# Kernel tuning notes

Hardware: AMD Instinct MI355X
Metric: run time of the kernel (lower is better)

## Reference

```python
import math
import jax, jax.numpy as jnp
import numpy as np

GRID = 16          # img_size // patch_size = 224 // 14
N_PER_H = 2048     # n_neurons // n_head = 8192 // 4
THETA = 10000.0


def _freqs_2d():
    """2D RoPE phase table, shape (1, 1, GRID*GRID, N_PER_H).
    Layout per position: [h_phases | w_phases | h_phases | w_phases], each half_dim//2 wide.
    """
    dim = N_PER_H
    half = dim // 2
    inv_freq = 1.0 / THETA ** (jnp.arange(0, half, 2, dtype=jnp.float32) / half)  # (half//2,)
    pos = jnp.arange(GRID, dtype=jnp.float32)
    ph = pos[:, None] * inv_freq[None, :]                       # (GRID, half//2)
    ph_h = jnp.broadcast_to(ph[:, None, :], (GRID, GRID, half // 2))
    ph_w = jnp.broadcast_to(ph[None, :, :], (GRID, GRID, half // 2))
    phases = jnp.concatenate([ph_h, ph_w, ph_h, ph_w], axis=-1)  # (GRID, GRID, dim)
    return phases.reshape(1, 1, GRID * GRID, dim)


def _rope(phases, v):
    ang = (phases % 1.0) * (2.0 * math.pi)
    c = jnp.cos(ang)
    s = jnp.sin(ang)
    # interleaved rotation: (-v_odd, v_even) re-interleaved
    v_rot = jnp.stack((-v[..., 1::2], v[..., ::2]), axis=-1).reshape(v.shape)
    return (v * c).astype(v.dtype) + (v_rot * s).astype(v.dtype)


def setup_inputs() -> dict:
    key = jax.random.key(0)
    kq, kk, kv = jax.random.split(key, 3)
    B, H, T, N = 16, 4, 256, N_PER_H
    D = 256
    Q = jax.random.normal(kq, (B, H, T, N), dtype=jnp.float32)
    K = jax.random.normal(kk, (B, H, T, N), dtype=jnp.float32)
    V = jax.random.normal(kv, (B, 1, T, D), dtype=jnp.float32)
    return {"Q": Q, "K": K, "V": V}


def reference(Q, K, V):
    B, H, T, N = Q.shape
    n_patches = GRID * GRID
    freqs = _freqs_2d()[:, :, :n_patches, :N]
    if T == n_patches + 1:  # static-shape branch (CLS token)
        Qr = jnp.concatenate([Q[:, :, :1, :], _rope(freqs, Q[:, :, 1:, :])], axis=2)
        Kr = jnp.concatenate([K[:, :, :1, :], _rope(freqs, K[:, :, 1:, :])], axis=2)
    else:
        f = freqs[:, :, :T, :]
        Qr = _rope(f, Q)
        Kr = _rope(f, K)
    # non-softmax bidirectional attention
    scores = jnp.einsum('bhtn,bhsn->bhts', Qr, Kr) / math.sqrt(N)  # (B,H,T,T)
    return jnp.matmul(scores, V)  # V (B,1,T,D) broadcasts over H -> (B,H,T,D)
```

## Files before the change

kernel.cpp:

```cpp
#include <hip/hip_runtime.h>
#include <hip/hip_bf16.h>

#define T_  256
#define NN_ 2048

typedef short bf16x8 __attribute__((ext_vector_type(8)));
typedef float f32x4  __attribute__((ext_vector_type(4)));
typedef unsigned u32x4 __attribute__((ext_vector_type(4)));

__device__ __forceinline__ unsigned short f2bf(float x) {
    union { float f; unsigned u; } v; v.f = x;
    unsigned r = v.u + 0x7fffu + ((v.u >> 16) & 1u);
    return (unsigned short)(r >> 16);
}
__device__ __forceinline__ float bflo(unsigned w) {
    union { unsigned u; float f; } v; v.u = w << 16; return v.f;
}
__device__ __forceinline__ float bfhi(unsigned w) {
    union { unsigned u; float f; } v; v.u = w & 0xffff0000u; return v.f;
}
__device__ __forceinline__ unsigned pkbf(float lo, float hi) {
    union { __hip_bfloat16 h; unsigned short s; } a, b;
    a.h = __float2bfloat16(lo);
    b.h = __float2bfloat16(hi);
    return (unsigned)a.s | ((unsigned)b.s << 16);
}

__device__ __forceinline__ void gld_lds16(const unsigned short* g, unsigned short* l) {
    __builtin_amdgcn_global_load_lds(
        (const __attribute__((address_space(1))) unsigned int*)g,
        (__attribute__((address_space(3))) unsigned int*)l, 16, 0, 0);
}

__global__ void prep(const float* __restrict__ V, unsigned short* __restrict__ Vt,
                     unsigned* __restrict__ cs) {
    const int tid = threadIdx.x;
    if (blockIdx.x >= 256) {
        int idx = (blockIdx.x - 256) * 256 + tid;
        int p = idx >> 9, f = idx & 511;
        float inv = powf(10000.0f, -(float)f * (1.0f / 512.0f));
        float ph  = (float)p * inv;
        float ang = (ph - floorf(ph)) * 6.28318530717958647692f;
        float s, c;
        sincosf(ang, &s, &c);
        cs[idx] = pkbf(c, s);
        return;
    }
    __shared__ unsigned short Tl[64 * 72];
    const int b  = blockIdx.x >> 4;
    const int s0 = ((blockIdx.x >> 2) & 3) << 6;
    const int d0 = (blockIdx.x & 3) << 6;
    const float* Vb = V + (size_t)b * 65536;
#pragma unroll
    for (int u = 0; u < 4; u++) {
        int lin = u * 256 + tid;
        int srow = lin >> 4, c4 = (lin & 15) << 2;
        float4 v = *(const float4*)(Vb + (size_t)(s0 + srow) * 256 + d0 + c4);
        Tl[(c4 + 0) * 72 + srow] = f2bf(v.x);
        Tl[(c4 + 1) * 72 + srow] = f2bf(v.y);
        Tl[(c4 + 2) * 72 + srow] = f2bf(v.z);
        Tl[(c4 + 3) * 72 + srow] = f2bf(v.w);
    }
    __syncthreads();
    unsigned short* Vtb = Vt + (size_t)b * 65536;
#pragma unroll
    for (int u = 0; u < 2; u++) {
        int lin = u * 256 + tid;
        int drow = lin >> 3, sc8 = (lin & 7) << 3;
        *(uint4*)(Vtb + (size_t)(d0 + drow) * 256 + s0 + sc8) =
            *(const uint4*)(&Tl[drow * 72 + sc8]);
    }
}

#define RSC 0.02209708691207961f

__launch_bounds__(256)
__global__ void rope_cast(const float* __restrict__ Q, const float* __restrict__ K,
                          const unsigned* __restrict__ cs,
                          unsigned short* __restrict__ Qr, unsigned short* __restrict__ Kr) {
    const size_t base = (size_t)blockIdx.x * 256 + threadIdx.x;
#pragma unroll
    for (int j = 0; j < 8; j++) {
        size_t o = base + (size_t)j * 1048576;
        const float* src;
        unsigned short* dst;
        float sc;
        if (j < 4) { src = Q; dst = Qr; sc = RSC; }
        else       { src = K; dst = Kr; sc = 1.0f; o -= 4194304; }
        const int t = (int)((o >> 8) & 255);
        const int w = (int)((o >> 6) & 1);
        const int f = ((int)o & 63) << 3;
        const int p = w ? (t & 15) : (t >> 4);
        const float* qp = src + o * 8;
        float4 q0 = *(const float4*)(qp);
        float4 q1 = *(const float4*)(qp + 4);
        const unsigned* cp = cs + (p << 9) + f;
        uint4 u0 = *(const uint4*)(cp);
        uint4 u1 = *(const uint4*)(cp + 4);
        q0.x *= sc; q0.y *= sc; q0.z *= sc; q0.w *= sc;
        q1.x *= sc; q1.y *= sc; q1.z *= sc; q1.w *= sc;
        u32x4 out;
        out[0] = pkbf(q0.x*bflo(u0.x) - q0.y*bfhi(u0.x),
                      q0.y*bflo(u0.y) + q0.x*bfhi(u0.y));
        out[1] = pkbf(q0.z*bflo(u0.z) - q0.w*bfhi(u0.z),
                      q0.w*bflo(u0.w) + q0.z*bfhi(u0.w));
        out[2] = pkbf(q1.x*bflo(u1.x) - q1.y*bfhi(u1.x),
                      q1.y*bflo(u1.y) + q1.x*bfhi(u1.y));
        out[3] = pkbf(q1.z*bflo(u1.z) - q1.w*bfhi(u1.z),
                      q1.w*bflo(u1.w) + q1.z*bfhi(u1.w));
        __builtin_nontemporal_store(out, (u32x4*)(dst + o * 8));
    }
}

__launch_bounds__(256)
__global__ void gemm1b(const unsigned short* __restrict__ Qr,
                       const unsigned short* __restrict__ Kr,
                       unsigned short* __restrict__ scores) {
    __shared__ __align__(16) unsigned short A[128 * 64];
    __shared__ __align__(16) unsigned short Bt[64 * 64];

    const int tid  = threadIdx.x;
    const int bh   = blockIdx.x & 63;
    const int tile = blockIdx.x >> 6;
    const int ti = (tile >> 2) << 7;
    const int si = (tile & 3) << 6;

    const unsigned short* Qb = Qr + (size_t)bh * (T_ * NN_);
    const unsigned short* Kb = Kr + (size_t)bh * (T_ * NN_);

    const unsigned short* srcA[4]; unsigned short* dstA[4];
    const unsigned short* srcB[2]; unsigned short* dstB[2];
#pragma unroll
    for (int u = 0; u < 4; u++) {
        int lin = u * 256 + tid;
        int row = lin >> 3, cu = lin & 7;
        int scol = cu ^ (row & 7);
        srcA[u] = Qb + (size_t)(ti + row) * NN_ + scol * 8;
        dstA[u] = &A[lin * 8];
    }
#pragma unroll
    for (int u = 0; u < 2; u++) {
        int lin = u * 256 + tid;
        int row = lin >> 3, cu = lin & 7;
        int scol = cu ^ (row & 7);
        srcB[u] = Kb + (size_t)(si + row) * NN_ + scol * 8;
        dstB[u] = &Bt[lin * 8];
    }

    const int wv = tid >> 6, lane = tid & 63;
    const int lr = lane & 15, lg = lane >> 4;
    const int m0 = (wv >> 1) * 64;
    const int n0 = (wv & 1) * 32;

    f32x4 acc[4][2];
#pragma unroll
    for (int i = 0; i < 4; i++)
#pragma unroll
        for (int j = 0; j < 2; j++) acc[i][j] = (f32x4){0.f, 0.f, 0.f, 0.f};

    for (int k0 = 0; k0 < NN_; k0 += 64) {
#pragma unroll
        for (int u = 0; u < 4; u++) gld_lds16(srcA[u] + k0, dstA[u]);
#pragma unroll
        for (int u = 0; u < 2; u++) gld_lds16(srcB[u] + k0, dstB[u]);
        __syncthreads();

#pragma unroll
        for (int kk = 0; kk < 64; kk += 32) {
            bf16x8 af[4], bfr[2];
#pragma unroll
            for (int mi = 0; mi < 4; mi++) {
                int row = m0 + mi * 16 + lr;
                int c   = (kk >> 3) + lg;
                af[mi] = *(const bf16x8*)(&A[row * 64 + ((c ^ (row & 7)) << 3)]);
            }
#pragma unroll
            for (int ni = 0; ni < 2; ni++) {
                int row = n0 + ni * 16 + lr;
                int c   = (kk >> 3) + lg;
                bfr[ni] = *(const bf16x8*)(&Bt[row * 64 + ((c ^ (row & 7)) << 3)]);
            }
#pragma unroll
            for (int mi = 0; mi < 4; mi++)
#pragma unroll
                for (int ni = 0; ni < 2; ni++)
                    acc[mi][ni] = __builtin_amdgcn_mfma_f32_16x16x32_bf16(
                        af[mi], bfr[ni], acc[mi][ni], 0, 0, 0);
        }
        __syncthreads();
    }

    unsigned short* sb = scores + (size_t)bh * (T_ * T_);
#pragma unroll
    for (int mi = 0; mi < 4; mi++) {
        int tr = ti + m0 + mi * 16 + lg * 4;
#pragma unroll
        for (int ni = 0; ni < 2; ni++) {
            int sc = si + n0 + ni * 16 + lr;
#pragma unroll
            for (int r = 0; r < 4; r++)
                sb[(size_t)(tr + r) * 256 + sc] = f2bf(acc[mi][ni][r]);
        }
    }
}

__launch_bounds__(256)
__global__ void gemm2b(const unsigned short* __restrict__ scores,
                       const unsigned short* __restrict__ Vt, float* __restrict__ out) {
    __shared__ __align__(16) unsigned short A[128 * 64];
    __shared__ __align__(16) unsigned short Bt[64 * 64];

    const int tid  = threadIdx.x;
    const int bh   = blockIdx.x & 63;
    const int b    = bh >> 2;
    const int tile = blockIdx.x >> 6;
    const int ti = (tile >> 2) << 7;
    const int d0 = (tile & 3) << 6;

    const unsigned short* Sb  = scores + (size_t)bh * 65536;
    const unsigned short* Vtb = Vt + (size_t)b * 65536;

    const unsigned short* srcA[4]; unsigned short* dstA[4];
    const unsigned short* srcB[2]; unsigned short* dstB[2];
#pragma unroll
    for (int u = 0; u < 4; u++) {
        int lin = u * 256 + tid;
        int row = lin >> 3, cu = lin & 7;
        int scol = cu ^ (row & 7);
        srcA[u] = Sb + (size_t)(ti + row) * 256 + scol * 8;
        dstA[u] = &A[lin * 8];
    }
#pragma unroll
    for (int u = 0; u < 2; u++) {
        int lin = u * 256 + tid;
        int row = lin >> 3, cu = lin & 7;
        int scol = cu ^ (row & 7);
        srcB[u] = Vtb + (size_t)(d0 + row) * 256 + scol * 8;
        dstB[u] = &Bt[lin * 8];
    }

    const int wv = tid >> 6, lane = tid & 63;
    const int lr = lane & 15, lg = lane >> 4;
    const int m0 = (wv >> 1) * 64;
    const int n0 = (wv & 1) * 32;

    f32x4 acc[4][2];
#pragma unroll
    for (int i = 0; i < 4; i++)
#pragma unroll
        for (int j = 0; j < 2; j++) acc[i][j] = (f32x4){0.f, 0.f, 0.f, 0.f};

    for (int k0 = 0; k0 < 256; k0 += 64) {
#pragma unroll
        for (int u = 0; u < 4; u++) gld_lds16(srcA[u] + k0, dstA[u]);
#pragma unroll
        for (int u = 0; u < 2; u++) gld_lds16(srcB[u] + k0, dstB[u]);
        __syncthreads();

#pragma unroll
        for (int kk = 0; kk < 64; kk += 32) {
            bf16x8 af[4], bfr[2];
#pragma unroll
            for (int mi = 0; mi < 4; mi++) {
                int row = m0 + mi * 16 + lr;
                int c   = (kk >> 3) + lg;
                af[mi] = *(const bf16x8*)(&A[row * 64 + ((c ^ (row & 7)) << 3)]);
            }
#pragma unroll
            for (int ni = 0; ni < 2; ni++) {
                int row = n0 + ni * 16 + lr;
                int c   = (kk >> 3) + lg;
                bfr[ni] = *(const bf16x8*)(&Bt[row * 64 + ((c ^ (row & 7)) << 3)]);
            }
#pragma unroll
            for (int mi = 0; mi < 4; mi++)
#pragma unroll
                for (int ni = 0; ni < 2; ni++)
                    acc[mi][ni] = __builtin_amdgcn_mfma_f32_16x16x32_bf16(
                        af[mi], bfr[ni], acc[mi][ni], 0, 0, 0);
        }
        __syncthreads();
    }

    float* ob = out + (size_t)bh * 65536;
#pragma unroll
    for (int mi = 0; mi < 4; mi++) {
        int tr = ti + m0 + mi * 16 + lg * 4;
#pragma unroll
        for (int ni = 0; ni < 2; ni++) {
            int dc = d0 + n0 + ni * 16 + lr;
#pragma unroll
            for (int r = 0; r < 4; r++)
                __builtin_nontemporal_store(acc[mi][ni][r],
                                            ob + (size_t)(tr + r) * 256 + dc);
        }
    }
}

extern "C" void kernel_launch(void* const* d_in, const int* in_sizes, int n_in,
                              void* d_out, int out_size, void* d_ws, size_t ws_size,
                              hipStream_t stream) {
    const float* Q = (const float*)d_in[0];
    const float* K = (const float*)d_in[1];
    const float* V = (const float*)d_in[2];
    float* out = (float*)d_out;

    unsigned* cs = (unsigned*)d_ws;
    unsigned short* scores = (unsigned short*)((char*)d_ws + 32768);
    unsigned short* Vt = (unsigned short*)((char*)d_ws + 32768 + 8388608);
    unsigned short* Qr = (unsigned short*)((char*)d_ws + 16777216);
    unsigned short* Kr = (unsigned short*)((char*)d_ws + 83886080);

    prep<<<dim3(288), dim3(256), 0, stream>>>(V, Vt, cs);
    rope_cast<<<dim3(4096), dim3(256), 0, stream>>>(Q, K, cs, Qr, Kr);
    gemm1b<<<dim3(512), dim3(256), 0, stream>>>(Qr, Kr, scores);
    gemm2b<<<dim3(512), dim3(256), 0, stream>>>(scores, Vt, out);
}
```

Before: 135.5 us.

## Fuse RoPE and bf16 cast into QK GEMM with double-buffered fp32 tiles

Drops the separate rope_cast kernel and its bf16 Qr/Kr round-trip through memory. The QK GEMM now loads fp32 Q/K tiles straight into LDS with double buffering, applies the rotation from an LDS-cached cos/sin table while building MFMA fragments, and applies the 1/sqrt(N) scale at the epilogue. Tiles become 128x128 with 512 threads, 256 blocks. In exchange the GEMM reads twice the bytes per element and does the rotation math in its inner loop, and there are fewer blocks to spread across the CUs.

```diff
diff --git a/kernel.cpp b/kernel.cpp
--- a/kernel.cpp
+++ b/kernel.cpp
@@ -3,6 +3,7 @@
 
 #define T_  256
 #define NN_ 2048
+#define RSC 0.02209708691207961f
 
 typedef short bf16x8 __attribute__((ext_vector_type(8)));
 typedef float f32x4  __attribute__((ext_vector_type(4)));
@@ -25,8 +26,7 @@
     b.h = __float2bfloat16(hi);
     return (unsigned)a.s | ((unsigned)b.s << 16);
 }
-
-__device__ __forceinline__ void gld_lds16(const unsigned short* g, unsigned short* l) {
+__device__ __forceinline__ void gld16(const void* g, void* l) {
     __builtin_amdgcn_global_load_lds(
         (const __attribute__((address_space(1))) unsigned int*)g,
         (__attribute__((address_space(3))) unsigned int*)l, 16, 0, 0);
@@ -72,85 +72,67 @@
     }
 }
 
-#define RSC 0.02209708691207961f
-
-__launch_bounds__(256)
-__global__ void rope_cast(const float* __restrict__ Q, const float* __restrict__ K,
-                          const unsigned* __restrict__ cs,
-                          unsigned short* __restrict__ Qr, unsigned short* __restrict__ Kr) {
-    const size_t base = (size_t)blockIdx.x * 256 + threadIdx.x;
-#pragma unroll
-    for (int j = 0; j < 8; j++) {
-        size_t o = base + (size_t)j * 1048576;
-        const float* src;
-        unsigned short* dst;
-        float sc;
-        if (j < 4) { src = Q; dst = Qr; sc = RSC; }
-        else       { src = K; dst = Kr; sc = 1.0f; o -= 4194304; }
-        const int t = (int)((o >> 8) & 255);
-        const int w = (int)((o >> 6) & 1);
-        const int f = ((int)o & 63) << 3;
-        const int p = w ? (t & 15) : (t >> 4);
-        const float* qp = src + o * 8;
-        float4 q0 = *(const float4*)(qp);
-        float4 q1 = *(const float4*)(qp + 4);
-        const unsigned* cp = cs + (p << 9) + f;
-        uint4 u0 = *(const uint4*)(cp);
-        uint4 u1 = *(const uint4*)(cp + 4);
-        q0.x *= sc; q0.y *= sc; q0.z *= sc; q0.w *= sc;
-        q1.x *= sc; q1.y *= sc; q1.z *= sc; q1.w *= sc;
-        u32x4 out;
-        out[0] = pkbf(q0.x*bflo(u0.x) - q0.y*bfhi(u0.x),
-                      q0.y*bflo(u0.y) + q0.x*bfhi(u0.y));
-        out[1] = pkbf(q0.z*bflo(u0.z) - q0.w*bfhi(u0.z),
-                      q0.w*bflo(u0.w) + q0.z*bfhi(u0.w));
-        out[2] = pkbf(q1.x*bflo(u1.x) - q1.y*bfhi(u1.x),
-                      q1.y*bflo(u1.y) + q1.x*bfhi(u1.y));
-        out[3] = pkbf(q1.z*bflo(u1.z) - q1.w*bfhi(u1.z),
-                      q1.w*bflo(u1.w) + q1.z*bfhi(u1.w));
-        __builtin_nontemporal_store(out, (u32x4*)(dst + o * 8));
-    }
-}
-
-__launch_bounds__(256)
-__global__ void gemm1b(const unsigned short* __restrict__ Qr,
-                       const unsigned short* __restrict__ Kr,
+__launch_bounds__(512)
+__global__ void gemm1f(const float* __restrict__ Q, const float* __restrict__ K,
+                       const unsigned* __restrict__ cs,
                        unsigned short* __restrict__ scores) {
-    __shared__ __align__(16) unsigned short A[128 * 64];
-    __shared__ __align__(16) unsigned short Bt[64 * 64];
-
-    const int tid  = threadIdx.x;
-    const int bh   = blockIdx.x & 63;
-    const int tile = blockIdx.x >> 6;
-    const int ti = (tile >> 2) << 7;
-    const int si = (tile & 3) << 6;
-
-    const unsigned short* Qb = Qr + (size_t)bh * (T_ * NN_);
-    const unsigned short* Kb = Kr + (size_t)bh * (T_ * NN_);
-
-    const unsigned short* srcA[4]; unsigned short* dstA[4];
-    const unsigned short* srcB[2]; unsigned short* dstB[2];
+    __shared__ __align__(16) float rawA[2][128 * 32];
+    __shared__ __align__(16) float rawB[2][128 * 32];
+    __shared__ __align__(16) unsigned csl[16 * 516];
+
+    const int tid = threadIdx.x;
+    const int bh  = blockIdx.x & 63;
+    const int qd  = blockIdx.x >> 6;
+    const int ti  = (qd >> 1) << 7;
+    const int si  = (qd & 1) << 7;
+
+    const float* Qb = Q + (size_t)bh * (T_ * NN_);
+    const float* Kb = K + (size_t)bh * (T_ * NN_);
+
+    const float* srcA[2]; int ldsA[2];
+    const float* srcB[2]; int ldsB[2];
+#pragma unroll
+    for (int u = 0; u < 2; u++) {
+        int lin = u * 512 + tid;
+        int row = lin >> 3, d = lin & 7;
+        int sg  = (d ^ (row & 7)) << 2;
+        srcA[u] = Qb + (size_t)(ti + row) * NN_ + sg;
+        srcB[u] = Kb + (size_t)(si + row) * NN_ + sg;
+        ldsA[u] = lin << 2;
+        ldsB[u] = lin << 2;
+    }
+    const unsigned* csrc[4]; int cdst[4];
 #pragma unroll
     for (int u = 0; u < 4; u++) {
-        int lin = u * 256 + tid;
-        int row = lin >> 3, cu = lin & 7;
-        int scol = cu ^ (row & 7);
-        srcA[u] = Qb + (size_t)(ti + row) * NN_ + scol * 8;
-        dstA[u] = &A[lin * 8];
-    }
-#pragma unroll
-    for (int u = 0; u < 2; u++) {
-        int lin = u * 256 + tid;
-        int row = lin >> 3, cu = lin & 7;
-        int scol = cu ^ (row & 7);
-        srcB[u] = Kb + (size_t)(si + row) * NN_ + scol * 8;
-        dstB[u] = &Bt[lin * 8];
+        int cu = u * 512 + tid;
+        int p = cu >> 7, fg = cu & 127;
+        csrc[u] = cs + (p << 9) + (fg << 2);
+        cdst[u] = p * 516 + (fg << 2);
     }
 
     const int wv = tid >> 6, lane = tid & 63;
     const int lr = lane & 15, lg = lane >> 4;
-    const int m0 = (wv >> 1) * 64;
-    const int n0 = (wv & 1) * 32;
+    const int m0 = (wv >> 2) * 64;
+    const int n0 = (wv & 3) * 32;
+
+    int offA0[4], offA1[4], pAh[4], pAw[4];
+#pragma unroll
+    for (int mi = 0; mi < 4; mi++) {
+        int row = m0 + mi * 16 + lr;
+        int gr  = ti + row;
+        offA0[mi] = row * 32 + ((( 2 * lg    ) ^ (row & 7)) << 2);
+        offA1[mi] = row * 32 + (((2 * lg + 1) ^ (row & 7)) << 2);
+        pAh[mi] = gr >> 4;  pAw[mi] = gr & 15;
+    }
+    int offB0[2], offB1[2], pBh[2], pBw[2];
+#pragma unroll
+    for (int ni = 0; ni < 2; ni++) {
+        int row = n0 + ni * 16 + lr;
+        int gr  = si + row;
+        offB0[ni] = row * 32 + ((( 2 * lg    ) ^ (row & 7)) << 2);
+        offB1[ni] = row * 32 + (((2 * lg + 1) ^ (row & 7)) << 2);
+        pBh[ni] = gr >> 4;  pBw[ni] = gr & 15;
+    }
 
     f32x4 acc[4][2];
 #pragma unroll
@@ -158,37 +140,78 @@
 #pragma unroll
         for (int j = 0; j < 2; j++) acc[i][j] = (f32x4){0.f, 0.f, 0.f, 0.f};
 
-    for (int k0 = 0; k0 < NN_; k0 += 64) {
-#pragma unroll
-        for (int u = 0; u < 4; u++) gld_lds16(srcA[u] + k0, dstA[u]);
-#pragma unroll
-        for (int u = 0; u < 2; u++) gld_lds16(srcB[u] + k0, dstB[u]);
-        __syncthreads();
-
-#pragma unroll
-        for (int kk = 0; kk < 64; kk += 32) {
-            bf16x8 af[4], bfr[2];
-#pragma unroll
-            for (int mi = 0; mi < 4; mi++) {
-                int row = m0 + mi * 16 + lr;
-                int c   = (kk >> 3) + lg;
-                af[mi] = *(const bf16x8*)(&A[row * 64 + ((c ^ (row & 7)) << 3)]);
-            }
-#pragma unroll
-            for (int ni = 0; ni < 2; ni++) {
-                int row = n0 + ni * 16 + lr;
-                int c   = (kk >> 3) + lg;
-                bfr[ni] = *(const bf16x8*)(&Bt[row * 64 + ((c ^ (row & 7)) << 3)]);
-            }
-#pragma unroll
-            for (int mi = 0; mi < 4; mi++)
-#pragma unroll
-                for (int ni = 0; ni < 2; ni++)
-                    acc[mi][ni] = __builtin_amdgcn_mfma_f32_16x16x32_bf16(
-                        af[mi], bfr[ni], acc[mi][ni], 0, 0, 0);
+    auto FRAG = [&](const float* rb, int o0, int o1, int p, int fb) -> bf16x8 {
+        float4 x0 = *(const float4*)(rb + o0);
+        float4 x1 = *(const float4*)(rb + o1);
+        const unsigned* ce = &csl[p * 516 + fb];
+        uint4 e0 = *(const uint4*)(ce);
+        uint4 e1 = *(const uint4*)(ce + 4);
+        union { u32x4 u; bf16x8 h; } o;
+        o.u[0] = pkbf(x0.x * bflo(e0.x) - x0.y * bfhi(e0.x),
+                      x0.y * bflo(e0.y) + x0.x * bfhi(e0.y));
+        o.u[1] = pkbf(x0.z * bflo(e0.z) - x0.w * bfhi(e0.z),
+                      x0.w * bflo(e0.w) + x0.z * bfhi(e0.w));
+        o.u[2] = pkbf(x1.x * bflo(e1.x) - x1.y * bfhi(e1.x),
+                      x1.y * bflo(e1.y) + x1.x * bfhi(e1.y));
+        o.u[3] = pkbf(x1.z * bflo(e1.z) - x1.w * bfhi(e1.z),
+                      x1.w * bflo(e1.w) + x1.z * bfhi(e1.w));
+        return o.h;
+    };
+
+#pragma unroll
+    for (int u = 0; u < 4; u++) gld16(csrc[u], &csl[cdst[u]]);
+#pragma unroll
+    for (int u = 0; u < 2; u++) {
+        gld16(srcA[u], &rawA[0][ldsA[u]]);
+        gld16(srcB[u], &rawB[0][ldsB[u]]);
+    }
+    asm volatile("s_waitcnt vmcnt(0)" ::: "memory");
+    __builtin_amdgcn_s_barrier();
+    asm volatile("" ::: "memory");
+
+#pragma unroll 1
+    for (int k = 0; k < 64; ++k) {
+        const int cur = k & 1;
+        const int kn  = (k < 63) ? (k + 1) : 63;
+#pragma unroll
+        for (int u = 0; u < 2; u++) {
+            gld16(srcA[u] + (kn << 5), &rawA[cur ^ 1][ldsA[u]]);
+            gld16(srcB[u] + (kn << 5), &rawB[cur ^ 1][ldsB[u]]);
         }
-        __syncthreads();
-    }
+        asm volatile("s_waitcnt vmcnt(4)" ::: "memory");
+        __builtin_amdgcn_s_barrier();
+        asm volatile("" ::: "memory");
+
+        const int k0 = k << 5;
+        const int fk = k0 & 511;
+        const int w  = (k0 >> 9) & 1;
+        const int fb = fk + lg * 8;
+
+        bf16x8 afr[4], bfr[2];
+#pragma unroll
+        for (int mi = 0; mi < 4; mi++)
+            afr[mi] = FRAG(&rawA[cur][0], offA0[mi], offA1[mi],
+                           w ? pAw[mi] : pAh[mi], fb);
+#pragma unroll
+        for (int ni = 0; ni < 2; ni++)
+            bfr[ni] = FRAG(&rawB[cur][0], offB0[ni], offB1[ni],
+                           w ? pBw[ni] : pBh[ni], fb);
+
+        __builtin_amdgcn_s_setprio(1);
+#pragma unroll
+        for (int mi = 0; mi < 4; mi++)
+#pragma unroll
+            for (int ni = 0; ni < 2; ni++)
+                acc[mi][ni] = __builtin_amdgcn_mfma_f32_16x16x32_bf16(
+                    afr[mi], bfr[ni], acc[mi][ni], 0, 0, 0);
+        __builtin_amdgcn_s_setprio(0);
+
+        asm volatile("s_waitcnt lgkmcnt(0)" ::: "memory");
+        __builtin_amdgcn_s_barrier();
+        asm volatile("" ::: "memory");
+    }
+
+    asm volatile("s_waitcnt vmcnt(0)" ::: "memory");
 
     unsigned short* sb = scores + (size_t)bh * (T_ * T_);
 #pragma unroll
@@ -199,7 +222,7 @@
             int sc = si + n0 + ni * 16 + lr;
 #pragma unroll
             for (int r = 0; r < 4; r++)
-                sb[(size_t)(tr + r) * 256 + sc] = f2bf(acc[mi][ni][r]);
+                sb[(size_t)(tr + r) * 256 + sc] = f2bf(acc[mi][ni][r] * RSC);
         }
     }
 }
@@ -252,9 +275,9 @@
 
     for (int k0 = 0; k0 < 256; k0 += 64) {
 #pragma unroll
-        for (int u = 0; u < 4; u++) gld_lds16(srcA[u] + k0, dstA[u]);
-#pragma unroll
-        for (int u = 0; u < 2; u++) gld_lds16(srcB[u] + k0, dstB[u]);
+        for (int u = 0; u < 4; u++) gld16(srcA[u] + k0, dstA[u]);
+#pragma unroll
+        for (int u = 0; u < 2; u++) gld16(srcB[u] + k0, dstB[u]);
         __syncthreads();
 
 #pragma unroll
@@ -308,11 +331,8 @@
     unsigned* cs = (unsigned*)d_ws;
     unsigned short* scores = (unsigned short*)((char*)d_ws + 32768);
     unsigned short* Vt = (unsigned short*)((char*)d_ws + 32768 + 8388608);
-    unsigned short* Qr = (unsigned short*)((char*)d_ws + 16777216);
-    unsigned short* Kr = (unsigned short*)((char*)d_ws + 83886080);
 
     prep<<<dim3(288), dim3(256), 0, stream>>>(V, Vt, cs);
-    rope_cast<<<dim3(4096), dim3(256), 0, stream>>>(Q, K, cs, Qr, Kr);
-    gemm1b<<<dim3(512), dim3(256), 0, stream>>>(Qr, Kr, scores);
+    gemm1f<<<dim3(256), dim3(512), 0, stream>>>(Q, K, cs, scores);
     gemm2b<<<dim3(512), dim3(256), 0, stream>>>(scores, Vt, out);
 }
```

Result: slower. 152.9 us (+12.8%).
